# Kernel tuning notes

Measured on AMD Instinct MI355X. Metric: run time of the kernel, lower is better.

Reference implementation:

```python
import jax, jax.numpy as jnp
import numpy as np

M_LEN = 1024
BATCH = 16384


def setup_inputs() -> dict:
    key = jax.random.key(0)
    k0, k1, k2, k3, kw = jax.random.split(key, 5)
    mod0 = jax.random.normal(k0, (BATCH, M_LEN), dtype=jnp.float32)
    mod1 = jax.random.normal(k1, (BATCH, M_LEN), dtype=jnp.float32)
    mod2 = jax.random.normal(k2, (BATCH, M_LEN), dtype=jnp.float32)
    mod3 = jax.random.normal(k3, (BATCH, M_LEN), dtype=jnp.float32)
    # simulate missing modality for first quarter of patients (exercises rescale path)
    mod1 = mod1.at[: BATCH // 4].set(0.0)
    W = jax.random.normal(kw, (M_LEN, M_LEN), dtype=jnp.float32) * (1.0 / np.sqrt(M_LEN))
    return {"mod0": mod0, "mod1": mod1, "mod2": mod2, "mod3": mod3, "W": W}


def reference(mod0, mod1, mod2, mod3, W):
    ndata = jnp.stack([mod0, mod1, mod2, mod3])          # [M, B, L]
    scores = jnp.einsum("mbl,kl->mbk", ndata, W)          # Linear (no bias): x @ W.T
    attention_weights = jax.nn.softmax(scores, axis=0)    # softmax over modalities
    fused = jnp.sum(ndata * attention_weights, axis=0)    # [B, L]
    # vectorized replacement of per-patient python loop:
    # count modalities whose sum is exactly zero; if >0, scale row by (count+1)
    zero_dims = jnp.sum(jnp.sum(ndata, axis=2) == 0.0, axis=0)          # [B] int
    scaler = jnp.where(zero_dims > 0, zero_dims + 1, 1).astype(fused.dtype)
    return fused * scaler[:, None]
```

## Files before the change

### kernel.cpp

```cpp
#include <hip/hip_runtime.h>
#include <hip/hip_bf16.h>

#define M_LEN 1024
#define BATCH 16384

#define BM 128
#define BN 128
#define BK 64
#define THREADS 256

typedef __attribute__((ext_vector_type(8))) short bf16x8;
typedef __attribute__((ext_vector_type(4))) float f32x4;
typedef unsigned short ushort_t;


__device__ __forceinline__ ushort_t bf16_rne(float f) {
    unsigned u = __float_as_uint(f);
    unsigned r = u + 0x7FFFu + ((u >> 16) & 1u);
    return (ushort_t)(r >> 16);
}

__device__ __forceinline__ float bf16_to_f(ushort_t u) {
    return __uint_as_float(((unsigned)u) << 16);
}

__device__ __forceinline__ unsigned pack2(float lo, float hi) {
    return __builtin_amdgcn_perm(__float_as_uint(hi), __float_as_uint(lo), 0x07060302u);
}

__device__ __forceinline__ void gload_lds16(const void* g, void* l) {
    __builtin_amdgcn_global_load_lds(
        (const __attribute__((address_space(1))) unsigned int*)g,
        (__attribute__((address_space(3))) unsigned int*)l,
        16, 0, 0);
}

__device__ __forceinline__ float4 ntload4(const float4* p) {
    f32x4 v = __builtin_nontemporal_load((const f32x4*)p);
    return make_float4(v.x, v.y, v.z, v.w);
}

__global__ __launch_bounds__(THREADS) void convert_pass(
    const float* __restrict__ mod0, const float* __restrict__ mod1,
    const float* __restrict__ mod2, const float* __restrict__ mod3,
    const float* __restrict__ W,
    ushort_t* __restrict__ Ab, ushort_t* __restrict__ Wb, int* __restrict__ zf)
{
    const int blk  = blockIdx.x;
    const int wave = threadIdx.x >> 6;
    const int lane = threadIdx.x & 63;

    if (blk < BATCH) {
        const int b = blk, m = wave;
        const float* mp = (m == 0) ? mod0 : (m == 1) ? mod1 : (m == 2) ? mod2 : mod3;
        const float4* row = (const float4*)(mp + (size_t)b * M_LEN);
        ushort_t* dst = Ab + ((size_t)b * 4 + m) * M_LEN;
        unsigned orr = 0u;
        #pragma unroll
        for (int j = 0; j < 4; ++j) {
            float4 v = ntload4(&row[j * 64 + lane]);
            orr |= (__float_as_uint(v.x) | __float_as_uint(v.y) |
                    __float_as_uint(v.z) | __float_as_uint(v.w)) << 1;
            ushort4 o;
            o.x = bf16_rne(v.x); o.y = bf16_rne(v.y);
            o.z = bf16_rne(v.z); o.w = bf16_rne(v.w);
            ((ushort4*)dst)[j * 64 + lane] = o;
        }
        const int nz = __any(orr != 0u);
        if (lane == 0) zf[b * 4 + m] = nz ? 0 : 1;
    } else {
        const int r = (blk - BATCH) * 4 + wave;
        const float4* row = (const float4*)(W + (size_t)r * M_LEN);
        ushort_t* dst = Wb + (size_t)r * M_LEN;
        #pragma unroll
        for (int j = 0; j < 4; ++j) {
            float4 v = row[j * 64 + lane];
            ushort4 o;
            o.x = bf16_rne(v.x); o.y = bf16_rne(v.y);
            o.z = bf16_rne(v.z); o.w = bf16_rne(v.w);
            ((ushort4*)dst)[j * 64 + lane] = o;
        }
    }
}

__global__ __launch_bounds__(THREADS) void gemm_fused(
    const ushort_t* __restrict__ Ab, const ushort_t* __restrict__ Wb,
    const int* __restrict__ zf, float* __restrict__ out)
{
    __shared__ __align__(16) ushort_t As[BM * BK];
    __shared__ __align__(16) ushort_t Bs[BN * BK];
    __shared__ float scalerS[BM / 4];

    const int t    = threadIdx.x;
    const int lane = t & 63;
    const int wave = t >> 6;
    const int quad = lane >> 4;
    const int ln15 = lane & 15;
    const int wm   = wave >> 1;
    const int wn   = wave & 1;

    const int colb = blockIdx.x;
    const int rowb = blockIdx.y;
    const int row0 = rowb * BM;
    const int col0 = colb * BN;

    if (t < 32) {
        const int4 f = ((const int4*)zf)[rowb * 32 + t];
        const int z = f.x + f.y + f.z + f.w;
        scalerS[t] = (z > 0) ? (float)(z + 1) : 1.0f;
    }

    const int rloc = (lane >> 3);
    const int c    = (lane & 7) ^ rloc;
    const ushort_t* aPtr[4];
    const ushort_t* bPtr[4];
    #pragma unroll
    for (int q = 0; q < 4; ++q) {
        const int r = wave * 32 + q * 8 + rloc;
        aPtr[q] = Ab + (size_t)(row0 + r) * M_LEN + c * 8;
        bPtr[q] = Wb + (size_t)(col0 + r) * M_LEN + c * 8;
    }

    f32x4 acc[4][4];
    #pragma unroll
    for (int i = 0; i < 4; ++i)
        #pragma unroll
        for (int j = 0; j < 4; ++j)
            acc[i][j] = (f32x4){0.f, 0.f, 0.f, 0.f};

    const unsigned slotB   = (unsigned)(quad ^ (ln15 & 7));
    const unsigned aRowOff = (unsigned)((wm * 64 + ln15) * 64);
    const unsigned bRowOff = (unsigned)((wn * 64 + ln15) * 64);

    for (int kt = 0; kt < 16; ++kt) {
        #pragma unroll
        for (int q = 0; q < 4; ++q) {
            gload_lds16(aPtr[q], &As[(wave * 4 + q) * 512]);
            gload_lds16(bPtr[q], &Bs[(wave * 4 + q) * 512]);
            aPtr[q] += BK;
            bPtr[q] += BK;
        }
        __syncthreads();
        #pragma unroll
        for (int ks = 0; ks < 2; ++ks) {
            const unsigned slot8 = (slotB ^ (unsigned)(ks * 4)) * 8u;
            bf16x8 af[4], bfr[4];
            #pragma unroll
            for (int i = 0; i < 4; ++i)
                af[i] = *(const bf16x8*)(&As[aRowOff + i * 1024 + slot8]);
            #pragma unroll
            for (int j = 0; j < 4; ++j)
                bfr[j] = *(const bf16x8*)(&Bs[bRowOff + j * 1024 + slot8]);
            #pragma unroll
            for (int i = 0; i < 4; ++i)
                #pragma unroll
                for (int j = 0; j < 4; ++j)
                    acc[i][j] = __builtin_amdgcn_mfma_f32_16x16x32_bf16(
                        af[i], bfr[j], acc[i][j], 0, 0, 0);
        }
        __syncthreads();
    }

    #pragma unroll
    for (int i = 0; i < 4; ++i) {
        const int bl = wm * 16 + i * 4 + quad;
        const int b  = rowb * 32 + bl;
        const float scal = scalerS[bl];
        const ushort_t* xr = Ab + (size_t)b * 4 * M_LEN;
        #pragma unroll
        for (int j = 0; j < 4; ++j) {
            const int k = col0 + wn * 64 + j * 16 + ln15;
            const float x0 = bf16_to_f(xr[k]);
            const float x1 = bf16_to_f(xr[M_LEN + k]);
            const float x2 = bf16_to_f(xr[2 * M_LEN + k]);
            const float x3 = bf16_to_f(xr[3 * M_LEN + k]);
            const f32x4 s = acc[i][j];
            const float mx = fmaxf(fmaxf(s.x, s.y), fmaxf(s.z, s.w));
            const float e0 = __expf(s.x - mx);
            const float e1 = __expf(s.y - mx);
            const float e2 = __expf(s.z - mx);
            const float e3 = __expf(s.w - mx);
            const float num = e0 * x0 + e1 * x1 + e2 * x2 + e3 * x3;
            const float v = num * scal / (e0 + e1 + e2 + e3);
            __builtin_nontemporal_store(v, &out[(size_t)b * M_LEN + k]);
        }
    }
}

__global__ __launch_bounds__(THREADS) void fused_modal_attn(
    const float* __restrict__ mod0, const float* __restrict__ mod1,
    const float* __restrict__ mod2, const float* __restrict__ mod3,
    const float* __restrict__ W, float* __restrict__ out)
{
    __shared__ __align__(16) unsigned short As[BM * BK];
    __shared__ __align__(16) unsigned short Bs[BN * BK];
    __shared__ unsigned rowOr[BM];
    __shared__ float scalerS[BM / 4];

    const int t    = threadIdx.x;
    const int lane = t & 63;
    const int wave = t >> 6;
    const int quad = lane >> 4;
    const int ln15 = lane & 15;
    const int wm   = wave >> 1;
    const int wn   = wave & 1;

    const int colb = blockIdx.x;
    const int rowb = blockIdx.y;
    const int row0 = rowb * BM;
    const int col0 = colb * BN;

    if (t < BM) rowOr[t] = 0u;

    const int sr  = t >> 3;
    const int scl = t & 7;

    const float* ap[4];
    const float* bp[4];
    unsigned ldsOff[4];
    unsigned orAcc[4] = {0u, 0u, 0u, 0u};
    #pragma unroll
    for (int j = 0; j < 4; ++j) {
        const int r  = j * 32 + sr;
        const int gr = row0 + r;
        const int b  = gr >> 2;
        const int m  = gr & 3;
        const float* mp = (m == 0) ? mod0 : (m == 1) ? mod1 : (m == 2) ? mod2 : mod3;
        ap[j] = mp + (size_t)b * M_LEN + scl * 8;
        bp[j] = W + (size_t)(col0 + r) * M_LEN + scl * 8;
        ldsOff[j] = (unsigned)(r * 64 + ((scl ^ (r & 7)) * 8));
    }

    f32x4 acc[4][4];
    #pragma unroll
    for (int i = 0; i < 4; ++i)
        #pragma unroll
        for (int j = 0; j < 4; ++j)
            acc[i][j] = (f32x4){0.f, 0.f, 0.f, 0.f};

    const unsigned slotB   = (unsigned)(quad ^ (ln15 & 7));
    const unsigned aRowOff = (unsigned)((wm * 64 + ln15) * 64);
    const unsigned bRowOff = (unsigned)((wn * 64 + ln15) * 64);

    for (int it = 0; it < 16; ++it) {
        __syncthreads();
        #pragma unroll
        for (int j = 0; j < 4; ++j) {
            const float4* pa = (const float4*)ap[j];
            const float4* pb = (const float4*)bp[j];
            float4 a0 = pa[0], a1 = pa[1];
            float4 b0 = pb[0], b1 = pb[1];
            ap[j] += BK; bp[j] += BK;

            unsigned pA0 = pack2(a0.x, a0.y), pA1 = pack2(a0.z, a0.w);
            unsigned pA2 = pack2(a1.x, a1.y), pA3 = pack2(a1.z, a1.w);
            orAcc[j] |= (pA0 | pA1) | (pA2 | pA3);
            *(uint4*)(&As[ldsOff[j]]) = make_uint4(pA0, pA1, pA2, pA3);

            unsigned pB0 = pack2(b0.x, b0.y), pB1 = pack2(b0.z, b0.w);
            unsigned pB2 = pack2(b1.x, b1.y), pB3 = pack2(b1.z, b1.w);
            *(uint4*)(&Bs[ldsOff[j]]) = make_uint4(pB0, pB1, pB2, pB3);
        }
        __syncthreads();
        #pragma unroll
        for (int ks = 0; ks < 2; ++ks) {
            const unsigned slot8 = (slotB ^ (unsigned)(ks * 4)) * 8u;
            bf16x8 af[4], bfr[4];
            #pragma unroll
            for (int i = 0; i < 4; ++i)
                af[i] = *(const bf16x8*)(&As[aRowOff + i * 1024 + slot8]);
            #pragma unroll
            for (int j = 0; j < 4; ++j)
                bfr[j] = *(const bf16x8*)(&Bs[bRowOff + j * 1024 + slot8]);
            #pragma unroll
            for (int i = 0; i < 4; ++i)
                #pragma unroll
                for (int j = 0; j < 4; ++j)
                    acc[i][j] = __builtin_amdgcn_mfma_f32_16x16x32_bf16(
                        af[i], bfr[j], acc[i][j], 0, 0, 0);
        }
    }

    #pragma unroll
    for (int j = 0; j < 4; ++j)
        atomicOr(&rowOr[j * 32 + sr], orAcc[j]);
    __syncthreads();
    if (t < 32) {
        const int z = (rowOr[4 * t + 0] == 0u) + (rowOr[4 * t + 1] == 0u)
                    + (rowOr[4 * t + 2] == 0u) + (rowOr[4 * t + 3] == 0u);
        scalerS[t] = (z > 0) ? (float)(z + 1) : 1.0f;
    }
    __syncthreads();

    #pragma unroll
    for (int i = 0; i < 4; ++i) {
        const int bl = wm * 16 + i * 4 + quad;
        const int b  = rowb * 32 + bl;
        const float scal = scalerS[bl];
        #pragma unroll
        for (int j = 0; j < 4; ++j) {
            const int k = col0 + wn * 64 + j * 16 + ln15;
            const size_t off = (size_t)b * M_LEN + k;
            const float x0 = mod0[off], x1 = mod1[off];
            const float x2 = mod2[off], x3 = mod3[off];
            const f32x4 s = acc[i][j];
            const float mx = fmaxf(fmaxf(s.x, s.y), fmaxf(s.z, s.w));
            const float e0 = __expf(s.x - mx);
            const float e1 = __expf(s.y - mx);
            const float e2 = __expf(s.z - mx);
            const float e3 = __expf(s.w - mx);
            const float num = e0 * x0 + e1 * x1 + e2 * x2 + e3 * x3;
            out[off] = num * scal / (e0 + e1 + e2 + e3);
        }
    }
}

extern "C" void kernel_launch(void* const* d_in, const int* in_sizes, int n_in,
                              void* d_out, int out_size, void* d_ws, size_t ws_size,
                              hipStream_t stream) {
    const float* mod0 = (const float*)d_in[0];
    const float* mod1 = (const float*)d_in[1];
    const float* mod2 = (const float*)d_in[2];
    const float* mod3 = (const float*)d_in[3];
    const float* W    = (const float*)d_in[4];
    float* out = (float*)d_out;

    const size_t abBytes = (size_t)4 * BATCH * M_LEN * sizeof(ushort_t);
    const size_t wbBytes = (size_t)M_LEN * M_LEN * sizeof(ushort_t);
    const size_t zfBytes = (size_t)4 * BATCH * sizeof(int);
    const size_t need = abBytes + wbBytes + zfBytes;

    if (ws_size >= need) {
        ushort_t* Ab = (ushort_t*)d_ws;
        ushort_t* Wb = (ushort_t*)((char*)d_ws + abBytes);
        int*      zfp = (int*)((char*)d_ws + abBytes + wbBytes);

        convert_pass<<<dim3(BATCH + M_LEN / 4), dim3(THREADS), 0, stream>>>(
            mod0, mod1, mod2, mod3, W, Ab, Wb, zfp);

        dim3 grid(M_LEN / BN, (4 * BATCH) / BM);
        gemm_fused<<<grid, dim3(THREADS), 0, stream>>>(Ab, Wb, zfp, out);
    } else {
        dim3 grid(M_LEN / BN, (4 * BATCH) / BM);
        fused_modal_attn<<<grid, dim3(THREADS), 0, stream>>>(
            mod0, mod1, mod2, mod3, W, out);
    }
}
```

Measured before the change: 410.8 us.

## Double-buffer LDS tiles in fused GEMM and remap blocks across XCDs

Shared-memory tiles for A and W are double-buffered, so the global-to-LDS load of the next K tile is issued before the MFMA work on the current tile, with one barrier per iteration instead of two. The grid becomes 1D, and block IDs are permuted so that consecutive hardware blocks (round-robined across the 8 XCDs) map to contiguous tile regions, aiming to improve L2 reuse. This doubles LDS use to 64KB per block, which may reduce occupancy.

```diff
diff --git a/kernel.cpp b/kernel.cpp
--- a/kernel.cpp
+++ b/kernel.cpp
@@ -87,8 +87,8 @@
     const ushort_t* __restrict__ Ab, const ushort_t* __restrict__ Wb,
     const int* __restrict__ zf, float* __restrict__ out)
 {
-    __shared__ __align__(16) ushort_t As[BM * BK];
-    __shared__ __align__(16) ushort_t Bs[BN * BK];
+    __shared__ __align__(16) ushort_t As[2][BM * BK];
+    __shared__ __align__(16) ushort_t Bs[2][BN * BK];
     __shared__ float scalerS[BM / 4];
 
     const int t    = threadIdx.x;
@@ -99,10 +99,31 @@
     const int wm   = wave >> 1;
     const int wn   = wave & 1;
 
-    const int colb = blockIdx.x;
-    const int rowb = blockIdx.y;
+    const int bid  = blockIdx.x;
+    const int wid  = (bid & 7) * 512 + (bid >> 3);
+    const int colb = wid & 7;
+    const int rowb = wid >> 3;
     const int row0 = rowb * BM;
     const int col0 = colb * BN;
+
+    const int rloc = (lane >> 3);
+    const int c    = (lane & 7) ^ rloc;
+    const ushort_t* aPtr[4];
+    const ushort_t* bPtr[4];
+    #pragma unroll
+    for (int q = 0; q < 4; ++q) {
+        const int r = wave * 32 + q * 8 + rloc;
+        aPtr[q] = Ab + (size_t)(row0 + r) * M_LEN + c * 8;
+        bPtr[q] = Wb + (size_t)(col0 + r) * M_LEN + c * 8;
+    }
+
+    #pragma unroll
+    for (int q = 0; q < 4; ++q) {
+        gload_lds16(aPtr[q], &As[0][(wave * 4 + q) * 512]);
+        gload_lds16(bPtr[q], &Bs[0][(wave * 4 + q) * 512]);
+        aPtr[q] += BK;
+        bPtr[q] += BK;
+    }
 
     if (t < 32) {
         const int4 f = ((const int4*)zf)[rowb * 32 + t];
@@ -110,17 +131,6 @@
         scalerS[t] = (z > 0) ? (float)(z + 1) : 1.0f;
     }
 
-    const int rloc = (lane >> 3);
-    const int c    = (lane & 7) ^ rloc;
-    const ushort_t* aPtr[4];
-    const ushort_t* bPtr[4];
-    #pragma unroll
-    for (int q = 0; q < 4; ++q) {
-        const int r = wave * 32 + q * 8 + rloc;
-        aPtr[q] = Ab + (size_t)(row0 + r) * M_LEN + c * 8;
-        bPtr[q] = Wb + (size_t)(col0 + r) * M_LEN + c * 8;
-    }
-
     f32x4 acc[4][4];
     #pragma unroll
     for (int i = 0; i < 4; ++i)
@@ -132,25 +142,29 @@
     const unsigned aRowOff = (unsigned)((wm * 64 + ln15) * 64);
     const unsigned bRowOff = (unsigned)((wn * 64 + ln15) * 64);
 
-    for (int kt = 0; kt < 16; ++kt) {
+    asm volatile("s_waitcnt vmcnt(0)" ::: "memory");
+    __builtin_amdgcn_s_barrier();
+
+    for (int kt = 0; kt < 15; ++kt) {
+        const int cur = kt & 1;
+        const int nxt = cur ^ 1;
         #pragma unroll
         for (int q = 0; q < 4; ++q) {
-            gload_lds16(aPtr[q], &As[(wave * 4 + q) * 512]);
-            gload_lds16(bPtr[q], &Bs[(wave * 4 + q) * 512]);
+            gload_lds16(aPtr[q], &As[nxt][(wave * 4 + q) * 512]);
+            gload_lds16(bPtr[q], &Bs[nxt][(wave * 4 + q) * 512]);
             aPtr[q] += BK;
             bPtr[q] += BK;
         }
-        __syncthreads();
         #pragma unroll
         for (int ks = 0; ks < 2; ++ks) {
             const unsigned slot8 = (slotB ^ (unsigned)(ks * 4)) * 8u;
             bf16x8 af[4], bfr[4];
             #pragma unroll
             for (int i = 0; i < 4; ++i)
-                af[i] = *(const bf16x8*)(&As[aRowOff + i * 1024 + slot8]);
+                af[i] = *(const bf16x8*)(&As[cur][aRowOff + i * 1024 + slot8]);
             #pragma unroll
             for (int j = 0; j < 4; ++j)
-                bfr[j] = *(const bf16x8*)(&Bs[bRowOff + j * 1024 + slot8]);
+                bfr[j] = *(const bf16x8*)(&Bs[cur][bRowOff + j * 1024 + slot8]);
             #pragma unroll
             for (int i = 0; i < 4; ++i)
                 #pragma unroll
@@ -158,7 +172,27 @@
                     acc[i][j] = __builtin_amdgcn_mfma_f32_16x16x32_bf16(
                         af[i], bfr[j], acc[i][j], 0, 0, 0);
         }
-        __syncthreads();
+        asm volatile("s_waitcnt lgkmcnt(0)" ::: "memory");
+        asm volatile("s_waitcnt vmcnt(0)" ::: "memory");
+        __builtin_amdgcn_s_barrier();
+    }
+
+    #pragma unroll
+    for (int ks = 0; ks < 2; ++ks) {
+        const unsigned slot8 = (slotB ^ (unsigned)(ks * 4)) * 8u;
+        bf16x8 af[4], bfr[4];
+        #pragma unroll
+        for (int i = 0; i < 4; ++i)
+            af[i] = *(const bf16x8*)(&As[1][aRowOff + i * 1024 + slot8]);
+        #pragma unroll
+        for (int j = 0; j < 4; ++j)
+            bfr[j] = *(const bf16x8*)(&Bs[1][bRowOff + j * 1024 + slot8]);
+        #pragma unroll
+        for (int i = 0; i < 4; ++i)
+            #pragma unroll
+            for (int j = 0; j < 4; ++j)
+                acc[i][j] = __builtin_amdgcn_mfma_f32_16x16x32_bf16(
+                    af[i], bfr[j], acc[i][j], 0, 0, 0);
     }
 
     #pragma unroll
@@ -338,8 +372,8 @@
         convert_pass<<<dim3(BATCH + M_LEN / 4), dim3(THREADS), 0, stream>>>(
             mod0, mod1, mod2, mod3, W, Ab, Wb, zfp);
 
-        dim3 grid(M_LEN / BN, (4 * BATCH) / BM);
-        gemm_fused<<<grid, dim3(THREADS), 0, stream>>>(Ab, Wb, zfp, out);
+        gemm_fused<<<dim3((M_LEN / BN) * ((4 * BATCH) / BM)), dim3(THREADS), 0, stream>>>(
+            Ab, Wb, zfp, out);
     } else {
         dim3 grid(M_LEN / BN, (4 * BATCH) / BM);
         fused_modal_attn<<<grid, dim3(THREADS), 0, stream>>>(
```

Result: slower. 428.8 us (+4.4%).

## Fuse activation bf16 conversion into GEMM and swizzle block order

Applied to the files above, without the earlier changes.

Drops the separate pass that converted all four modality inputs to bf16 in a workspace. The GEMM now loads fp32 activations directly, converts them in registers, writes them to LDS, and tracks zero rows with per-row OR reductions. A 1D grid with a block-index remap makes the eight column blocks that share one row block run adjacently, so they can reuse activations from L2. In exchange, every activation element is now converted eight times (once per column block), and the A loads are synchronous register loads instead of async LDS loads, which can stall the MFMA loop.

```diff
diff --git a/kernel.cpp b/kernel.cpp
--- a/kernel.cpp
+++ b/kernel.cpp
@@ -18,10 +18,6 @@
     unsigned u = __float_as_uint(f);
     unsigned r = u + 0x7FFFu + ((u >> 16) & 1u);
     return (ushort_t)(r >> 16);
-}
-
-__device__ __forceinline__ float bf16_to_f(ushort_t u) {
-    return __uint_as_float(((unsigned)u) << 16);
 }
 
 __device__ __forceinline__ unsigned pack2(float lo, float hi) {
@@ -35,60 +31,32 @@
         16, 0, 0);
 }
 
-__device__ __forceinline__ float4 ntload4(const float4* p) {
-    f32x4 v = __builtin_nontemporal_load((const f32x4*)p);
-    return make_float4(v.x, v.y, v.z, v.w);
-}
-
-__global__ __launch_bounds__(THREADS) void convert_pass(
+__global__ __launch_bounds__(THREADS) void convert_w(
+    const float* __restrict__ W, ushort_t* __restrict__ Wb)
+{
+    const int wave = threadIdx.x >> 6;
+    const int lane = threadIdx.x & 63;
+    const int r = blockIdx.x * 4 + wave;
+    const float4* row = (const float4*)(W + (size_t)r * M_LEN);
+    ushort_t* dst = Wb + (size_t)r * M_LEN;
+    #pragma unroll
+    for (int j = 0; j < 4; ++j) {
+        float4 v = row[j * 64 + lane];
+        ushort4 o;
+        o.x = bf16_rne(v.x); o.y = bf16_rne(v.y);
+        o.z = bf16_rne(v.z); o.w = bf16_rne(v.w);
+        ((ushort4*)dst)[j * 64 + lane] = o;
+    }
+}
+
+__global__ __launch_bounds__(THREADS) void gemm_fused2(
     const float* __restrict__ mod0, const float* __restrict__ mod1,
     const float* __restrict__ mod2, const float* __restrict__ mod3,
-    const float* __restrict__ W,
-    ushort_t* __restrict__ Ab, ushort_t* __restrict__ Wb, int* __restrict__ zf)
-{
-    const int blk  = blockIdx.x;
-    const int wave = threadIdx.x >> 6;
-    const int lane = threadIdx.x & 63;
-
-    if (blk < BATCH) {
-        const int b = blk, m = wave;
-        const float* mp = (m == 0) ? mod0 : (m == 1) ? mod1 : (m == 2) ? mod2 : mod3;
-        const float4* row = (const float4*)(mp + (size_t)b * M_LEN);
-        ushort_t* dst = Ab + ((size_t)b * 4 + m) * M_LEN;
-        unsigned orr = 0u;
-        #pragma unroll
-        for (int j = 0; j < 4; ++j) {
-            float4 v = ntload4(&row[j * 64 + lane]);
-            orr |= (__float_as_uint(v.x) | __float_as_uint(v.y) |
-                    __float_as_uint(v.z) | __float_as_uint(v.w)) << 1;
-            ushort4 o;
-            o.x = bf16_rne(v.x); o.y = bf16_rne(v.y);
-            o.z = bf16_rne(v.z); o.w = bf16_rne(v.w);
-            ((ushort4*)dst)[j * 64 + lane] = o;
-        }
-        const int nz = __any(orr != 0u);
-        if (lane == 0) zf[b * 4 + m] = nz ? 0 : 1;
-    } else {
-        const int r = (blk - BATCH) * 4 + wave;
-        const float4* row = (const float4*)(W + (size_t)r * M_LEN);
-        ushort_t* dst = Wb + (size_t)r * M_LEN;
-        #pragma unroll
-        for (int j = 0; j < 4; ++j) {
-            float4 v = row[j * 64 + lane];
-            ushort4 o;
-            o.x = bf16_rne(v.x); o.y = bf16_rne(v.y);
-            o.z = bf16_rne(v.z); o.w = bf16_rne(v.w);
-            ((ushort4*)dst)[j * 64 + lane] = o;
-        }
-    }
-}
-
-__global__ __launch_bounds__(THREADS) void gemm_fused(
-    const ushort_t* __restrict__ Ab, const ushort_t* __restrict__ Wb,
-    const int* __restrict__ zf, float* __restrict__ out)
+    const ushort_t* __restrict__ Wb, float* __restrict__ out)
 {
     __shared__ __align__(16) ushort_t As[BM * BK];
     __shared__ __align__(16) ushort_t Bs[BN * BK];
+    __shared__ unsigned rowOr[BM];
     __shared__ float scalerS[BM / 4];
 
     const int t    = threadIdx.x;
@@ -99,26 +67,38 @@
     const int wm   = wave >> 1;
     const int wn   = wave & 1;
 
-    const int colb = blockIdx.x;
-    const int rowb = blockIdx.y;
+    const int bid  = blockIdx.x;
+    const int wid  = (bid & 7) * 512 + (bid >> 3);
+    const int colb = wid & 7;
+    const int rowb = wid >> 3;
     const int row0 = rowb * BM;
     const int col0 = colb * BN;
 
-    if (t < 32) {
-        const int4 f = ((const int4*)zf)[rowb * 32 + t];
-        const int z = f.x + f.y + f.z + f.w;
-        scalerS[t] = (z > 0) ? (float)(z + 1) : 1.0f;
+    if (t < BM) rowOr[t] = 0u;
+
+    const int sr  = t >> 3;
+    const int scl = t & 7;
+    const float* ap[4];
+    unsigned ldsOffA[4];
+    unsigned orAcc[4] = {0u, 0u, 0u, 0u};
+    #pragma unroll
+    for (int j = 0; j < 4; ++j) {
+        const int r  = j * 32 + sr;
+        const int gr = row0 + r;
+        const int b  = gr >> 2;
+        const int m  = gr & 3;
+        const float* mp = (m == 0) ? mod0 : (m == 1) ? mod1 : (m == 2) ? mod2 : mod3;
+        ap[j] = mp + (size_t)b * M_LEN + scl * 8;
+        ldsOffA[j] = (unsigned)(r * 64 + ((scl ^ (r & 7)) * 8));
     }
 
     const int rloc = (lane >> 3);
-    const int c    = (lane & 7) ^ rloc;
-    const ushort_t* aPtr[4];
+    const int cB   = (lane & 7) ^ rloc;
     const ushort_t* bPtr[4];
     #pragma unroll
     for (int q = 0; q < 4; ++q) {
         const int r = wave * 32 + q * 8 + rloc;
-        aPtr[q] = Ab + (size_t)(row0 + r) * M_LEN + c * 8;
-        bPtr[q] = Wb + (size_t)(col0 + r) * M_LEN + c * 8;
+        bPtr[q] = Wb + (size_t)(col0 + r) * M_LEN + cB * 8;
     }
 
     f32x4 acc[4][4];
@@ -132,15 +112,42 @@
     const unsigned aRowOff = (unsigned)((wm * 64 + ln15) * 64);
     const unsigned bRowOff = (unsigned)((wn * 64 + ln15) * 64);
 
-    for (int kt = 0; kt < 16; ++kt) {
+    for (int it = 0; it < 16; ++it) {
+        __syncthreads();
+
         #pragma unroll
         for (int q = 0; q < 4; ++q) {
-            gload_lds16(aPtr[q], &As[(wave * 4 + q) * 512]);
             gload_lds16(bPtr[q], &Bs[(wave * 4 + q) * 512]);
-            aPtr[q] += BK;
             bPtr[q] += BK;
         }
+
+        float4 a0[4], a1[4];
+        #pragma unroll
+        for (int j = 0; j < 4; ++j) {
+            const float4* pa = (const float4*)ap[j];
+            a0[j] = pa[0];
+            a1[j] = pa[1];
+            ap[j] += BK;
+        }
+        #pragma unroll
+        for (int j = 0; j < 4; ++j) {
+            const unsigned w0 = __float_as_uint(a0[j].x) | __float_as_uint(a0[j].y) |
+                                __float_as_uint(a0[j].z) | __float_as_uint(a0[j].w);
+            const unsigned w1 = __float_as_uint(a1[j].x) | __float_as_uint(a1[j].y) |
+                                __float_as_uint(a1[j].z) | __float_as_uint(a1[j].w);
+            orAcc[j] |= (w0 | w1) << 1;
+            ushort4 lo, hi;
+            lo.x = bf16_rne(a0[j].x); lo.y = bf16_rne(a0[j].y);
+            lo.z = bf16_rne(a0[j].z); lo.w = bf16_rne(a0[j].w);
+            hi.x = bf16_rne(a1[j].x); hi.y = bf16_rne(a1[j].y);
+            hi.z = bf16_rne(a1[j].z); hi.w = bf16_rne(a1[j].w);
+            ushort4* dst = (ushort4*)&As[ldsOffA[j]];
+            dst[0] = lo;
+            dst[1] = hi;
+        }
+
         __syncthreads();
+
         #pragma unroll
         for (int ks = 0; ks < 2; ++ks) {
             const unsigned slot8 = (slotB ^ (unsigned)(ks * 4)) * 8u;
@@ -158,22 +165,30 @@
                     acc[i][j] = __builtin_amdgcn_mfma_f32_16x16x32_bf16(
                         af[i], bfr[j], acc[i][j], 0, 0, 0);
         }
-        __syncthreads();
-    }
+    }
+
+    #pragma unroll
+    for (int j = 0; j < 4; ++j)
+        atomicOr(&rowOr[j * 32 + sr], orAcc[j]);
+    __syncthreads();
+    if (t < 32) {
+        const int z = (rowOr[4 * t + 0] == 0u) + (rowOr[4 * t + 1] == 0u)
+                    + (rowOr[4 * t + 2] == 0u) + (rowOr[4 * t + 3] == 0u);
+        scalerS[t] = (z > 0) ? (float)(z + 1) : 1.0f;
+    }
+    __syncthreads();
 
     #pragma unroll
     for (int i = 0; i < 4; ++i) {
         const int bl = wm * 16 + i * 4 + quad;
         const int b  = rowb * 32 + bl;
         const float scal = scalerS[bl];
-        const ushort_t* xr = Ab + (size_t)b * 4 * M_LEN;
         #pragma unroll
         for (int j = 0; j < 4; ++j) {
             const int k = col0 + wn * 64 + j * 16 + ln15;
-            const float x0 = bf16_to_f(xr[k]);
-            const float x1 = bf16_to_f(xr[M_LEN + k]);
-            const float x2 = bf16_to_f(xr[2 * M_LEN + k]);
-            const float x3 = bf16_to_f(xr[3 * M_LEN + k]);
+            const size_t off = (size_t)b * M_LEN + k;
+            const float x0 = mod0[off], x1 = mod1[off];
+            const float x2 = mod2[off], x3 = mod3[off];
             const f32x4 s = acc[i][j];
             const float mx = fmaxf(fmaxf(s.x, s.y), fmaxf(s.z, s.w));
             const float e0 = __expf(s.x - mx);
@@ -182,7 +197,7 @@
             const float e3 = __expf(s.w - mx);
             const float num = e0 * x0 + e1 * x1 + e2 * x2 + e3 * x3;
             const float v = num * scal / (e0 + e1 + e2 + e3);
-            __builtin_nontemporal_store(v, &out[(size_t)b * M_LEN + k]);
+            __builtin_nontemporal_store(v, &out[off]);
         }
     }
 }
@@ -325,21 +340,13 @@
     const float* W    = (const float*)d_in[4];
     float* out = (float*)d_out;
 
-    const size_t abBytes = (size_t)4 * BATCH * M_LEN * sizeof(ushort_t);
     const size_t wbBytes = (size_t)M_LEN * M_LEN * sizeof(ushort_t);
-    const size_t zfBytes = (size_t)4 * BATCH * sizeof(int);
-    const size_t need = abBytes + wbBytes + zfBytes;
-
-    if (ws_size >= need) {
-        ushort_t* Ab = (ushort_t*)d_ws;
-        ushort_t* Wb = (ushort_t*)((char*)d_ws + abBytes);
-        int*      zfp = (int*)((char*)d_ws + abBytes + wbBytes);
-
-        convert_pass<<<dim3(BATCH + M_LEN / 4), dim3(THREADS), 0, stream>>>(
-            mod0, mod1, mod2, mod3, W, Ab, Wb, zfp);
-
-        dim3 grid(M_LEN / BN, (4 * BATCH) / BM);
-        gemm_fused<<<grid, dim3(THREADS), 0, stream>>>(Ab, Wb, zfp, out);
+
+    if (ws_size >= wbBytes) {
+        ushort_t* Wb = (ushort_t*)d_ws;
+        convert_w<<<dim3(M_LEN / 4), dim3(THREADS), 0, stream>>>(W, Wb);
+        gemm_fused2<<<dim3((M_LEN / BN) * ((4 * BATCH) / BM)), dim3(THREADS), 0, stream>>>(
+            mod0, mod1, mod2, mod3, Wb, out);
     } else {
         dim3 grid(M_LEN / BN, (4 * BATCH) / BM);
         fused_modal_attn<<<grid, dim3(THREADS), 0, stream>>>(
```

New measurement: 491.1 us. 19.5% more time.

## Use 256x256 tiles with double-buffered LDS and swizzled block order in fused GEMM

Applied to the files above, without the earlier changes.

Replaces the 128x128 single-buffered GEMM with a 256x256 tile computed by 512 threads. Two LDS buffers let global-to-LDS loads of the next K-slice overlap MFMA work, using explicit vmcnt waits and barriers in place of __syncthreads. Blocks are remapped onto a 1D grid with an XCD-aware swizzle to improve L2 reuse. The larger tile raises data reuse per load, at the cost of more registers (32 accumulators per thread) and 128KB of LDS per block, which may limit occupancy.

```diff
diff --git a/kernel.cpp b/kernel.cpp
--- a/kernel.cpp
+++ b/kernel.cpp
@@ -8,6 +8,10 @@
 #define BN 128
 #define BK 64
 #define THREADS 256
+
+#define BM2 256
+#define BN2 256
+#define GTHREADS 512
 
 typedef __attribute__((ext_vector_type(8))) short bf16x8;
 typedef __attribute__((ext_vector_type(4))) float f32x4;
@@ -83,88 +87,123 @@
     }
 }
 
-__global__ __launch_bounds__(THREADS) void gemm_fused(
+__global__ __launch_bounds__(GTHREADS, 2) void gemm_fused3(
     const ushort_t* __restrict__ Ab, const ushort_t* __restrict__ Wb,
     const int* __restrict__ zf, float* __restrict__ out)
 {
-    __shared__ __align__(16) ushort_t As[BM * BK];
-    __shared__ __align__(16) ushort_t Bs[BN * BK];
-    __shared__ float scalerS[BM / 4];
+    __shared__ __align__(16) ushort_t As0[BM2 * BK];
+    __shared__ __align__(16) ushort_t Bs0[BN2 * BK];
+    __shared__ __align__(16) ushort_t As1[BM2 * BK];
+    __shared__ __align__(16) ushort_t Bs1[BN2 * BK];
+    __shared__ float scalerS[BM2 / 4];
 
     const int t    = threadIdx.x;
     const int lane = t & 63;
     const int wave = t >> 6;
     const int quad = lane >> 4;
     const int ln15 = lane & 15;
-    const int wm   = wave >> 1;
-    const int wn   = wave & 1;
-
-    const int colb = blockIdx.x;
-    const int rowb = blockIdx.y;
-    const int row0 = rowb * BM;
-    const int col0 = colb * BN;
-
-    if (t < 32) {
-        const int4 f = ((const int4*)zf)[rowb * 32 + t];
+    const int wm   = wave >> 2;
+    const int wn   = wave & 3;
+
+    const int bid  = blockIdx.x;
+    const int wid  = (bid & 7) * 128 + (bid >> 3);
+    const int colb = wid & 3;
+    const int rowb = wid >> 2;
+    const int row0 = rowb * BM2;
+    const int col0 = colb * BN2;
+
+    if (t < 64) {
+        const int4 f = ((const int4*)zf)[rowb * 64 + t];
         const int z = f.x + f.y + f.z + f.w;
         scalerS[t] = (z > 0) ? (float)(z + 1) : 1.0f;
     }
 
     const int rloc = (lane >> 3);
-    const int c    = (lane & 7) ^ rloc;
-    const ushort_t* aPtr[4];
-    const ushort_t* bPtr[4];
+    const int c8   = (lane & 7) ^ rloc;
+    const ushort_t* aP[4];
+    const ushort_t* bP[4];
+    unsigned dstOff[4];
     #pragma unroll
     for (int q = 0; q < 4; ++q) {
         const int r = wave * 32 + q * 8 + rloc;
-        aPtr[q] = Ab + (size_t)(row0 + r) * M_LEN + c * 8;
-        bPtr[q] = Wb + (size_t)(col0 + r) * M_LEN + c * 8;
-    }
-
-    f32x4 acc[4][4];
-    #pragma unroll
-    for (int i = 0; i < 4; ++i)
+        aP[q] = Ab + (size_t)(row0 + r) * M_LEN + c8 * 8;
+        bP[q] = Wb + (size_t)(col0 + r) * M_LEN + c8 * 8;
+        dstOff[q] = (unsigned)((wave * 32 + q * 8) * 64);
+    }
+
+    #define STAGE(AD, BD)                                                   \
+        do {                                                                \
+            _Pragma("unroll")                                               \
+            for (int q = 0; q < 4; ++q) {                                   \
+                gload_lds16(aP[q], (AD) + dstOff[q]);                       \
+                aP[q] += BK;                                                \
+            }                                                               \
+            _Pragma("unroll")                                               \
+            for (int q = 0; q < 4; ++q) {                                   \
+                gload_lds16(bP[q], (BD) + dstOff[q]);                       \
+                bP[q] += BK;                                                \
+            }                                                               \
+        } while (0)
+
+    f32x4 acc[8][4];
+    #pragma unroll
+    for (int i = 0; i < 8; ++i)
         #pragma unroll
         for (int j = 0; j < 4; ++j)
             acc[i][j] = (f32x4){0.f, 0.f, 0.f, 0.f};
 
     const unsigned slotB   = (unsigned)(quad ^ (ln15 & 7));
-    const unsigned aRowOff = (unsigned)((wm * 64 + ln15) * 64);
+    const unsigned aRowOff = (unsigned)((wm * 128 + ln15) * 64);
     const unsigned bRowOff = (unsigned)((wn * 64 + ln15) * 64);
 
-    for (int kt = 0; kt < 16; ++kt) {
-        #pragma unroll
-        for (int q = 0; q < 4; ++q) {
-            gload_lds16(aPtr[q], &As[(wave * 4 + q) * 512]);
-            gload_lds16(bPtr[q], &Bs[(wave * 4 + q) * 512]);
-            aPtr[q] += BK;
-            bPtr[q] += BK;
-        }
-        __syncthreads();
+    auto compute = [&](const ushort_t* As_, const ushort_t* Bs_) {
         #pragma unroll
         for (int ks = 0; ks < 2; ++ks) {
             const unsigned slot8 = (slotB ^ (unsigned)(ks * 4)) * 8u;
-            bf16x8 af[4], bfr[4];
-            #pragma unroll
-            for (int i = 0; i < 4; ++i)
-                af[i] = *(const bf16x8*)(&As[aRowOff + i * 1024 + slot8]);
+            bf16x8 af[8], bfr[4];
+            #pragma unroll
+            for (int i = 0; i < 8; ++i)
+                af[i] = *(const bf16x8*)(&As_[aRowOff + i * 1024 + slot8]);
             #pragma unroll
             for (int j = 0; j < 4; ++j)
-                bfr[j] = *(const bf16x8*)(&Bs[bRowOff + j * 1024 + slot8]);
-            #pragma unroll
-            for (int i = 0; i < 4; ++i)
+                bfr[j] = *(const bf16x8*)(&Bs_[bRowOff + j * 1024 + slot8]);
+            #pragma unroll
+            for (int i = 0; i < 8; ++i)
                 #pragma unroll
                 for (int j = 0; j < 4; ++j)
                     acc[i][j] = __builtin_amdgcn_mfma_f32_16x16x32_bf16(
                         af[i], bfr[j], acc[i][j], 0, 0, 0);
         }
-        __syncthreads();
-    }
-
-    #pragma unroll
-    for (int i = 0; i < 4; ++i) {
-        const int bl = wm * 16 + i * 4 + quad;
-        const int b  = rowb * 32 + bl;
+    };
+
+    STAGE(As0, Bs0);
+    STAGE(As1, Bs1);
+    asm volatile("s_waitcnt vmcnt(8) lgkmcnt(0)" ::: "memory");
+    __builtin_amdgcn_s_barrier();
+
+    #pragma unroll 1
+    for (int t2 = 0; t2 < 7; ++t2) {
+        compute(As0, Bs0);
+        __builtin_amdgcn_s_barrier();
+        STAGE(As0, Bs0);
+        asm volatile("s_waitcnt vmcnt(8)" ::: "memory");
+        __builtin_amdgcn_s_barrier();
+
+        compute(As1, Bs1);
+        __builtin_amdgcn_s_barrier();
+        STAGE(As1, Bs1);
+        asm volatile("s_waitcnt vmcnt(8)" ::: "memory");
+        __builtin_amdgcn_s_barrier();
+    }
+    compute(As0, Bs0);
+    asm volatile("s_waitcnt vmcnt(0)" ::: "memory");
+    __builtin_amdgcn_s_barrier();
+    compute(As1, Bs1);
+
+    #pragma unroll
+    for (int i = 0; i < 8; ++i) {
+        const int bl = wm * 32 + i * 4 + quad;
+        const int b  = rowb * 64 + bl;
         const float scal = scalerS[bl];
         const ushort_t* xr = Ab + (size_t)b * 4 * M_LEN;
         #pragma unroll
@@ -185,6 +224,7 @@
             __builtin_nontemporal_store(v, &out[(size_t)b * M_LEN + k]);
         }
     }
+    #undef STAGE
 }
 
 __global__ __launch_bounds__(THREADS) void fused_modal_attn(
@@ -338,8 +378,8 @@
         convert_pass<<<dim3(BATCH + M_LEN / 4), dim3(THREADS), 0, stream>>>(
             mod0, mod1, mod2, mod3, W, Ab, Wb, zfp);
 
-        dim3 grid(M_LEN / BN, (4 * BATCH) / BM);
-        gemm_fused<<<grid, dim3(THREADS), 0, stream>>>(Ab, Wb, zfp, out);
+        gemm_fused3<<<dim3((M_LEN / BN2) * ((4 * BATCH) / BM2)), dim3(GTHREADS), 0, stream>>>(
+            Ab, Wb, zfp, out);
     } else {
         dim3 grid(M_LEN / BN, (4 * BATCH) / BM);
         fused_modal_attn<<<grid, dim3(THREADS), 0, stream>>>(
```

After: 384.2 us. 1.07x faster.
